# Kernel tuning notes

Measured on AMD Instinct MI355X. Metric: run time of the kernel, lower is better.

Reference implementation:

```python
import jax, jax.numpy as jnp
import numpy as np

NEG_INF = -1e30
EPS = 1e-6


def _apply_rope_interleaved(x, cos, sin):
    # x: (..., rope_dim); cos/sin broadcastable to (..., rope_dim//2)
    x1 = x[..., 0::2]
    x2 = x[..., 1::2]
    o1 = x1 * cos - x2 * sin
    o2 = x1 * sin + x2 * cos
    return jnp.stack([o1, o2], axis=-1).reshape(x.shape)


def setup_inputs() -> dict:
    key = jax.random.key(0)
    ks = jax.random.split(key, 6)
    B, S, D = 1, 2048, 7168
    H, HD, ROPE, QLR = 64, 128, 64, 1536
    x = jax.random.normal(ks[0], (B, S, D), dtype=jnp.float32)
    q_lora = jax.random.normal(ks[1], (B, S, QLR), dtype=jnp.float32)
    wq_b = jax.random.normal(ks[2], (QLR, H * HD), dtype=jnp.float32) * 0.02
    wk = jax.random.normal(ks[3], (D, HD), dtype=jnp.float32) * 0.02
    weights_proj = jax.random.normal(ks[4], (D, H), dtype=jnp.float32) * 0.02
    k_norm_w = jnp.ones((HD,), dtype=jnp.float32)
    k_norm_b = jnp.zeros((HD,), dtype=jnp.float32)
    # standard RoPE tables for the first ROPE dims
    half = ROPE // 2
    inv_freq = 1.0 / (10000.0 ** (np.arange(half, dtype=np.float64) / half))
    ang = np.arange(S, dtype=np.float64)[:, None] * inv_freq[None, :]
    cos = jnp.asarray(np.cos(ang), dtype=jnp.float32)
    sin = jnp.asarray(np.sin(ang), dtype=jnp.float32)
    return {"x": x, "q_lora": q_lora, "wq_b": wq_b, "wk": wk,
            "weights_proj": weights_proj, "k_norm_w": k_norm_w,
            "k_norm_b": k_norm_b, "cos": cos, "sin": sin, "topk": 512}


def reference(x, q_lora, wq_b, wk, weights_proj, k_norm_w, k_norm_b, cos, sin, topk):
    B, S, D = x.shape
    HD = wk.shape[1]
    H = weights_proj.shape[1]
    ROPE = cos.shape[1] * 2
    # queries: low-rank up-projection -> per-head, RoPE on first ROPE dims
    q = (q_lora @ wq_b).reshape(B, S, H, HD)
    q_pe = _apply_rope_interleaved(q[..., :ROPE], cos[None, :, None, :], sin[None, :, None, :])
    q = jnp.concatenate([q_pe, q[..., ROPE:]], axis=-1)
    # keys: single head, LayerNorm then RoPE on first ROPE dims
    k = x @ wk  # [B,S,HD]
    mu = k.mean(-1, keepdims=True)
    var = ((k - mu) ** 2).mean(-1, keepdims=True)
    k = (k - mu) * jax.lax.rsqrt(var + EPS) * k_norm_w + k_norm_b
    k_pe = _apply_rope_interleaved(k[..., :ROPE], cos[None], sin[None])
    k = jnp.concatenate([k_pe, k[..., ROPE:]], axis=-1)
    # per-token head gates, scaled by n_heads^-0.5 and softmax scale HD^-0.5
    w = (x @ weights_proj) * (H ** -0.5) * (HD ** -0.5)  # [B,S,H]
    # lightning index score: I[t,s] = sum_h w[t,h] * relu(q[t,h] . k[s])
    scores = jax.nn.relu(jnp.einsum('bshd,btd->bsht', q, k))  # [B,S,H,S]
    index_score = jnp.einsum('bsht,bsh->bst', scores, w)      # [B,S,S]
    # causal mask then top-k token selection
    causal = jnp.arange(S)[None, :] <= jnp.arange(S)[:, None]
    index_score = jnp.where(causal[None], index_score, NEG_INF)
    vals, idx = jax.lax.top_k(index_score, topk)
    return vals, idx
```

## Files before the change

### kernel.cpp

```cpp
#include <hip/hip_runtime.h>
#include <stdint.h>

#define S_LEN 2048
#define D_DIM 7168
#define H_NUM 64
#define HD_DIM 128
#define QLR_DIM 1536
#define NQ_DIM 8192
#define ROPE_DIM 64
#define HALF_DIM 32
#define TOPK_N 512
#define NEG_INF_F (-1e30f)
#define LN_EPS 1e-6f
#define W_SCALE 0.011048543456039806f

#define KCHUNKS 7
#define KCHUNK_SZ 1024
#define NKT 24

#define QF_HSTRIDE (128 * 4 * 64 * 8)

#define QBF_OFF 0
#define ALORA_OFF (QBF_OFF + S_LEN * NQ_DIM / 2)
#define WT_OFF   (ALORA_OFF + S_LEN * QLR_DIM / 2)
#define XBF_OFF  (WT_OFF + NQ_DIM * QLR_DIM / 2)
#define WT2_OFF  (XBF_OFF + S_LEN * D_DIM / 2)
#define KF_OFF   (WT2_OFF + 192 * D_DIM / 2)
#define KBF_OFF  (KF_OFF + S_LEN * HD_DIM)
#define WF_OFF   (KBF_OFF + S_LEN * HD_DIM / 2)
#define SC_OFF   (WF_OFF + S_LEN * H_NUM)

typedef __attribute__((ext_vector_type(8))) short short8;
typedef __attribute__((ext_vector_type(4))) float floatx4;

__device__ __forceinline__ ushort f2bf(float f) {
    unsigned int u = __float_as_uint(f);
    u += 0x7FFFu + ((u >> 16) & 1u);
    return (ushort)(u >> 16);
}
__device__ __forceinline__ unsigned int pack2bf(float lo, float hi) {
    return (unsigned int)f2bf(lo) | ((unsigned int)f2bf(hi) << 16);
}

__device__ __forceinline__ void gld_lds16(const ushort* g, ushort* l) {
    __builtin_amdgcn_global_load_lds(
        (const __attribute__((address_space(1))) unsigned int*)g,
        (__attribute__((address_space(3))) unsigned int*)l, 16, 0, 0);
}

__global__ __launch_bounds__(256) void cast_bf16_kernel(
    const float* __restrict__ in, ushort* __restrict__ out)
{
    int g = (blockIdx.x * 256 + threadIdx.x) * 8;
    float4 a = *(const float4*)&in[g];
    float4 b = *(const float4*)&in[g + 4];
    uint4 v;
    v.x = pack2bf(a.x, a.y); v.y = pack2bf(a.z, a.w);
    v.z = pack2bf(b.x, b.y); v.w = pack2bf(b.z, b.w);
    *(uint4*)&out[g] = v;
}

__global__ __launch_bounds__(256) void transpose_wqb_kernel(
    const float* __restrict__ W, ushort* __restrict__ WT)
{
    __shared__ ushort tl[64][72];
    const int n0 = blockIdx.x * 64, k0 = blockIdx.y * 64;
    const int t = threadIdx.x;
    const int r = t >> 4, c4 = (t & 15) * 4;
#pragma unroll
    for (int u = 0; u < 4; u++) {
        int kk = r + u * 16;
        float4 v = *(const float4*)&W[(size_t)(k0 + kk) * NQ_DIM + n0 + c4];
        tl[c4 + 0][kk] = f2bf(v.x);
        tl[c4 + 1][kk] = f2bf(v.y);
        tl[c4 + 2][kk] = f2bf(v.z);
        tl[c4 + 3][kk] = f2bf(v.w);
    }
    __syncthreads();
#pragma unroll
    for (int u = 0; u < 2; u++) {
        int i = t + u * 256;
        int nr = i >> 3, c8 = (i & 7) * 8;
        uint4 v = *(const uint4*)&tl[nr][c8];
        *(uint4*)&WT[(size_t)(n0 + nr) * QLR_DIM + k0 + c8] = v;
    }
}

__global__ __launch_bounds__(256) void transpose_wkp_kernel(
    const float* __restrict__ WK, const float* __restrict__ WP,
    ushort* __restrict__ WT2)
{
    __shared__ ushort tl[64][72];
    const int ntile = blockIdx.x;
    const int k0 = blockIdx.y * 64;
    const float* src; int ld, cbase;
    if (ntile < 2) { src = WK; ld = HD_DIM; cbase = ntile * 64; }
    else           { src = WP; ld = H_NUM; cbase = 0; }
    const int t = threadIdx.x;
    const int r = t >> 4, c4 = (t & 15) * 4;
#pragma unroll
    for (int u = 0; u < 4; u++) {
        int kk = r + u * 16;
        float4 v = *(const float4*)&src[(size_t)(k0 + kk) * ld + cbase + c4];
        tl[c4 + 0][kk] = f2bf(v.x);
        tl[c4 + 1][kk] = f2bf(v.y);
        tl[c4 + 2][kk] = f2bf(v.z);
        tl[c4 + 3][kk] = f2bf(v.w);
    }
    __syncthreads();
#pragma unroll
    for (int u = 0; u < 2; u++) {
        int i = t + u * 256;
        int nr = i >> 3, c8 = (i & 7) * 8;
        uint4 v = *(const uint4*)&tl[nr][c8];
        *(uint4*)&WT2[(size_t)(ntile * 64 + nr) * D_DIM + k0 + c8] = v;
    }
}

__global__ __launch_bounds__(512, 2) void qgemm_mfma_kernel(
    const ushort* __restrict__ Abf,
    const ushort* __restrict__ WT,
    const float* __restrict__ cosp, const float* __restrict__ sinp,
    ushort* __restrict__ Qo)
{
    __shared__ __align__(16) ushort lds[65536];

    const int tid = threadIdx.x;
    const int lane = tid & 63;
    const int wave = tid >> 6;
    const int m = lane & 15;
    const int q = lane >> 4;
    const int wm = wave & 1;
    const int wn = wave >> 1;

    const int wg = blockIdx.x;
    const int xcd = wg & 7, lid = wg >> 3;
    const int bx = xcd * 4 + (lid & 3);
    const int by = lid >> 2;
    const int m0 = by * 256;
    const int n0 = bx * 256;

    const ushort* sgA[2][2];
    const ushort* sgB[2][2];
    unsigned int ldoff[2][2];
#pragma unroll
    for (int h = 0; h < 2; h++)
#pragma unroll
        for (int r = 0; r < 2; r++) {
            int s = r * 512 + wave * 64 + lane;
            int row = s >> 3, c = s & 7;
            int kg = c ^ (row & 7);
            sgA[h][r] = Abf + (size_t)(m0 + h * 128 + row) * QLR_DIM + kg * 8;
            sgB[h][r] = WT  + (size_t)(n0 + h * 128 + row) * QLR_DIM + kg * 8;
            ldoff[h][r] = (unsigned int)(h * 8192 + (r * 512 + wave * 64) * 8);
        }

    auto stageA = [&](int kt, int h) {
        ushort* dbase = &lds[(kt & 1) * 16384];
        gld_lds16(sgA[h][0] + kt * 64, dbase + ldoff[h][0]);
        gld_lds16(sgA[h][1] + kt * 64, dbase + ldoff[h][1]);
    };
    auto stageB = [&](int kt, int h) {
        ushort* dbase = &lds[32768 + (kt & 1) * 16384];
        gld_lds16(sgB[h][0] + kt * 64, dbase + ldoff[h][0]);
        gld_lds16(sgB[h][1] + kt * 64, dbase + ldoff[h][1]);
    };

    unsigned int aoff[2], boff[2];
#pragma unroll
    for (int ks = 0; ks < 2; ks++) {
        unsigned int xr = (unsigned int)(((((ks << 2) + q) ^ (m & 7))) * 8);
        aoff[ks] = (unsigned int)((wm * 128 + m) * 64) + xr;
        boff[ks] = (unsigned int)((wn * 64 + m) * 64) + xr;
    }

    floatx4 acc[8][4];
#pragma unroll
    for (int i = 0; i < 8; i++)
#pragma unroll
        for (int j = 0; j < 4; j++) acc[i][j] = (floatx4){0.f, 0.f, 0.f, 0.f};

    stageA(0, 0); stageA(0, 1); stageB(0, 0); stageB(0, 1);
    asm volatile("s_waitcnt vmcnt(0)" ::: "memory");
    __builtin_amdgcn_s_barrier();

#pragma unroll 2
    for (int kt = 0; kt < NKT; ++kt) {
        const ushort* as = &lds[(kt & 1) * 16384];
        const ushort* bs = &lds[32768 + (kt & 1) * 16384];
        const bool pf = (kt + 1 < NKT);

        short8 af[4], bf0[4], bf1[4];

#pragma unroll
        for (int mt = 0; mt < 4; mt++)
            af[mt] = *(const short8*)&as[aoff[0] + mt * 1024];
#pragma unroll
        for (int nt = 0; nt < 4; nt++)
            bf0[nt] = *(const short8*)&bs[boff[0] + nt * 1024];
        if (pf) { stageA(kt + 1, 0); stageA(kt + 1, 1); stageB(kt + 1, 0); }
        __builtin_amdgcn_s_barrier();
        __builtin_amdgcn_s_setprio(1);
#pragma unroll
        for (int mt = 0; mt < 4; mt++)
#pragma unroll
            for (int nt = 0; nt < 4; nt++)
                acc[mt][nt] = __builtin_amdgcn_mfma_f32_16x16x32_bf16(
                    af[mt], bf0[nt], acc[mt][nt], 0, 0, 0);
        __builtin_amdgcn_s_setprio(0);
        __builtin_amdgcn_s_barrier();

#pragma unroll
        for (int mt = 0; mt < 4; mt++)
            af[mt] = *(const short8*)&as[aoff[1] + mt * 1024];
#pragma unroll
        for (int nt = 0; nt < 4; nt++)
            bf1[nt] = *(const short8*)&bs[boff[1] + nt * 1024];
        if (pf) stageB(kt + 1, 1);
        __builtin_amdgcn_s_barrier();
        __builtin_amdgcn_s_setprio(1);
#pragma unroll
        for (int mt = 0; mt < 4; mt++)
#pragma unroll
            for (int nt = 0; nt < 4; nt++)
                acc[mt][nt] = __builtin_amdgcn_mfma_f32_16x16x32_bf16(
                    af[mt], bf1[nt], acc[mt][nt], 0, 0, 0);
        __builtin_amdgcn_s_setprio(0);
        __builtin_amdgcn_s_barrier();

#pragma unroll
        for (int mt = 0; mt < 4; mt++)
            af[mt] = *(const short8*)&as[aoff[0] + 4096 + mt * 1024];
        __builtin_amdgcn_s_barrier();
        __builtin_amdgcn_s_setprio(1);
#pragma unroll
        for (int mt = 0; mt < 4; mt++)
#pragma unroll
            for (int nt = 0; nt < 4; nt++)
                acc[4 + mt][nt] = __builtin_amdgcn_mfma_f32_16x16x32_bf16(
                    af[mt], bf0[nt], acc[4 + mt][nt], 0, 0, 0);
        __builtin_amdgcn_s_setprio(0);
        __builtin_amdgcn_s_barrier();

#pragma unroll
        for (int mt = 0; mt < 4; mt++)
            af[mt] = *(const short8*)&as[aoff[1] + 4096 + mt * 1024];
        __builtin_amdgcn_s_barrier();
        __builtin_amdgcn_s_setprio(1);
#pragma unroll
        for (int mt = 0; mt < 4; mt++)
#pragma unroll
            for (int nt = 0; nt < 4; nt++)
                acc[4 + mt][nt] = __builtin_amdgcn_mfma_f32_16x16x32_bf16(
                    af[mt], bf1[nt], acc[4 + mt][nt], 0, 0, 0);
        __builtin_amdgcn_s_setprio(0);
        asm volatile("s_waitcnt vmcnt(0)" ::: "memory");
        __builtin_amdgcn_s_barrier();
    }

    __syncthreads();
    ushort* ep = lds;
    const int h0 = bx * 2;
    const int sgrp0 = m0 >> 4;

#pragma unroll
    for (int hh = 0; hh < 2; hh++) {
        if ((wn >> 1) == hh) {
            const int dbase = (wn & 1) * 64;
            const bool do_rope = ((wn & 1) == 0);
#pragma unroll
            for (int ai = 0; ai < 8; ai++) {
                const int srow0 = m0 + wm * 128 + ai * 16 + q * 4;
#pragma unroll
                for (int bj = 0; bj < 4; bj++) {
                    const int d = dbase + bj * 16 + m;
                    float o[4];
                    if (do_rope) {
                        const int jj = d >> 1;
#pragma unroll
                        for (int r = 0; r < 4; r++) {
                            float x = acc[ai][bj][r];
                            float p = __shfl_xor(x, 1, 64);
                            float c = cosp[(srow0 + r) * HALF_DIM + jj];
                            float sn = sinp[(srow0 + r) * HALF_DIM + jj];
                            o[r] = (d & 1) ? (p * sn + x * c) : (x * c - p * sn);
                        }
                    } else {
#pragma unroll
                        for (int r = 0; r < 4; r++) o[r] = acc[ai][bj][r];
                    }
#pragma unroll
                    for (int r = 0; r < 4; r++)
                        ep[(wm * 128 + ai * 16 + q * 4 + r) * 136 + d] = f2bf(o[r]);
                }
            }
        }
        __syncthreads();
        const size_t hstr = (size_t)(h0 + hh) * QF_HSTRIDE;
#pragma unroll
        for (int u = 0; u < 8; u++) {
            int i = u * 512 + tid;
            int sgl = i >> 8, c = i & 255;
            int ks = c >> 6, ln = c & 63;
            int srow = sgl * 16 + (ln & 15);
            int d0 = (ks << 5) + ((ln >> 4) << 3);
            uint4 v = *(const uint4*)&ep[srow * 136 + d0];
            *(uint4*)&Qo[hstr + ((((size_t)(sgrp0 + sgl) * 4 + ks) * 64 + ln) * 8)] = v;
        }
        __syncthreads();
    }
}

__global__ __launch_bounds__(256) void kw_mfma_kernel(
    const ushort* __restrict__ Xbf,
    const ushort* __restrict__ WT2,
    float* __restrict__ partial)
{
    __shared__ ushort As[128 * 64];
    __shared__ ushort Bs[64 * 64];

    const int tid = threadIdx.x;
    const int lane = tid & 63;
    const int wave = tid >> 6;
    const int m = lane & 15;
    const int q = lane >> 4;
    const int wm = wave & 1, wn = wave >> 1;
    const int m0 = blockIdx.x * 128;
    const int n0 = blockIdx.y * 64;
    const int kc = blockIdx.z;
    const size_t kbase = (size_t)kc * KCHUNK_SZ;

    const ushort* agp[4];
    unsigned int abase[4];
#pragma unroll
    for (int u = 0; u < 4; u++) {
        int s = (u * 4 + wave) * 64 + lane;
        int row = s >> 3, c = s & 7;
        int kg = c ^ (row & 7);
        agp[u] = Xbf + (size_t)(m0 + row) * D_DIM + kbase + kg * 8;
        abase[u] = (unsigned int)((u * 4 + wave) * 64 * 8);
    }
    const ushort* bgp[2];
    unsigned int bbase[2];
#pragma unroll
    for (int u = 0; u < 2; u++) {
        int s = (u * 4 + wave) * 64 + lane;
        int row = s >> 3, c = s & 7;
        int kg = c ^ (row & 7);
        bgp[u] = WT2 + (size_t)(n0 + row) * D_DIM + kbase + kg * 8;
        bbase[u] = (unsigned int)((u * 4 + wave) * 64 * 8);
    }

    floatx4 acc[4][2];
#pragma unroll
    for (int i = 0; i < 4; i++)
#pragma unroll
        for (int j = 0; j < 2; j++) acc[i][j] = (floatx4){0.f, 0.f, 0.f, 0.f};

    for (int kt = 0; kt < KCHUNK_SZ; kt += 64) {
        __syncthreads();
#pragma unroll
        for (int u = 0; u < 4; u++) gld_lds16(agp[u] + kt, &As[abase[u]]);
#pragma unroll
        for (int u = 0; u < 2; u++) gld_lds16(bgp[u] + kt, &Bs[bbase[u]]);
        __syncthreads();

        short8 af[4][2], bfr[2][2];
#pragma unroll
        for (int mt = 0; mt < 4; mt++) {
            int row = wm * 64 + mt * 16 + m;
#pragma unroll
            for (int ks = 0; ks < 2; ks++)
                af[mt][ks] = *(const short8*)
                    &As[row * 64 + ((((ks << 2) + q) ^ (m & 7)) * 8)];
        }
#pragma unroll
        for (int nt = 0; nt < 2; nt++) {
            int row = wn * 32 + nt * 16 + m;
#pragma unroll
            for (int ks = 0; ks < 2; ks++)
                bfr[nt][ks] = *(const short8*)
                    &Bs[row * 64 + ((((ks << 2) + q) ^ (m & 7)) * 8)];
        }
#pragma unroll
        for (int mt = 0; mt < 4; mt++)
#pragma unroll
            for (int nt = 0; nt < 2; nt++)
#pragma unroll
                for (int ks = 0; ks < 2; ks++)
                    acc[mt][nt] = __builtin_amdgcn_mfma_f32_16x16x32_bf16(
                        af[mt][ks], bfr[nt][ks], acc[mt][nt], 0, 0, 0);
    }

#pragma unroll
    for (int mt = 0; mt < 4; mt++) {
        int grow = m0 + wm * 64 + mt * 16 + q * 4;
#pragma unroll
        for (int nt = 0; nt < 2; nt++) {
            int gn = n0 + wn * 32 + nt * 16 + m;
#pragma unroll
            for (int r = 0; r < 4; r++)
                partial[((size_t)kc * S_LEN + grow + r) * 192 + gn] = acc[mt][nt][r];
        }
    }
}

__global__ __launch_bounds__(256) void kw_reduce_kernel(
    const float* __restrict__ partial, float* __restrict__ Ko, float* __restrict__ Wo)
{
    int g = blockIdx.x * 256 + threadIdx.x;
    int m = g / 192, n = g % 192;
    float s = 0.f;
#pragma unroll
    for (int c = 0; c < KCHUNKS; c++)
        s += partial[((size_t)c * S_LEN + m) * 192 + n];
    if (n < HD_DIM) Ko[(size_t)m * HD_DIM + n] = s;
    else            Wo[(size_t)m * H_NUM + (n - HD_DIM)] = s * W_SCALE;
}

__global__ __launch_bounds__(128) void knorm_rope_kernel(
    const float* __restrict__ Kf, const float* __restrict__ gw, const float* __restrict__ gb,
    const float* __restrict__ cosp, const float* __restrict__ sinp,
    ushort* __restrict__ Kbf)
{
    __shared__ float red[128];
    __shared__ float sh[128];
    const int m = blockIdx.x, t = threadIdx.x;
    float v = Kf[(size_t)m * HD_DIM + t];
    red[t] = v; __syncthreads();
    for (int off = 64; off > 0; off >>= 1) {
        if (t < off) red[t] += red[t + off];
        __syncthreads();
    }
    float mu = red[0] * (1.f / HD_DIM);
    __syncthreads();
    float dv = v - mu;
    red[t] = dv * dv; __syncthreads();
    for (int off = 64; off > 0; off >>= 1) {
        if (t < off) red[t] += red[t + off];
        __syncthreads();
    }
    float var = red[0] * (1.f / HD_DIM);
    float rs = rsqrtf(var + LN_EPS);
    float kn = dv * rs * gw[t] + gb[t];
    sh[t] = kn; __syncthreads();
    float out;
    if (t < ROPE_DIM) {
        int jj = t >> 1;
        float c = cosp[m * HALF_DIM + jj], sn = sinp[m * HALF_DIM + jj];
        out = ((t & 1) == 0) ? (sh[t] * c - sh[t + 1] * sn)
                             : (sh[t - 1] * sn + sh[t] * c);
    } else {
        out = kn;
    }
    Kbf[(size_t)m * HD_DIM + t] = f2bf(out);
}

__global__ __launch_bounds__(256, 2) void attn_mfma_kernel(
    const ushort* __restrict__ Qb,
    const ushort* __restrict__ Kb,
    const float* __restrict__ Wf,
    float* __restrict__ SC)
{
    __shared__ float Wsm[64 * 68];

    const int bidx = blockIdx.x;
    const int x = bidx & 7, j = bidx >> 3;
    const int g1 = x + 1, g2 = 32 - x, g3 = x + 9;
    int ts, tt;
    if (j < g1)                { ts = x;      tt = j; }
    else if (j < g1 + g2)      { ts = 31 - x; tt = j - g1; }
    else if (j < g1 + g2 + g3) { ts = x + 8;  tt = j - g1 - g2; }
    else                       { ts = 23 - x; tt = j - g1 - g2 - g3; }
    const int s0 = ts * 64, t0 = tt * 64;

    const int tid = threadIdx.x;
    const int lane = tid & 63;
    const int m = lane & 15;
    const int q = lane >> 4;
    const int strip = (tid >> 6) * 16;

    {
        const float4* gw = (const float4*)(Wf + (size_t)s0 * H_NUM);
#pragma unroll
        for (int u = 0; u < 4; u++) {
            int ch = tid + u * 256;
            float4 v = gw[ch];
            *(float4*)&Wsm[(ch >> 4) * 68 + (ch & 15) * 4] = v;
        }
    }

    short8 bf[4][4];
#pragma unroll
    for (int tile = 0; tile < 4; tile++)
#pragma unroll
        for (int ks = 0; ks < 4; ks++)
            bf[tile][ks] = *(const short8*)
                &Kb[(size_t)(t0 + tile * 16 + m) * HD_DIM + ks * 32 + q * 8];

    __syncthreads();

    float acc[4][4];
#pragma unroll
    for (int tile = 0; tile < 4; tile++)
#pragma unroll
        for (int r = 0; r < 4; r++) acc[tile][r] = 0.f;

    const int sgrp = ts * 4 + (strip >> 4);
    const ushort* qfb = Qb + ((size_t)sgrp * 4 * 64 + lane) * 8;
    const float* wrow = &Wsm[(strip + q * 4) * 68];

    auto loadQ = [&](short8* dst, int h) {
        const ushort* p = qfb + (size_t)h * QF_HSTRIDE;
#pragma unroll
        for (int ks = 0; ks < 4; ks++) dst[ks] = *(const short8*)&p[ks * 512];
    };
    auto computeH = [&](const short8* af, int h) {
        float wv[4];
#pragma unroll
        for (int r = 0; r < 4; r++) wv[r] = wrow[r * 68 + h];
#pragma unroll
        for (int tile = 0; tile < 4; tile++) {
            floatx4 p = {0.f, 0.f, 0.f, 0.f};
#pragma unroll
            for (int ks = 0; ks < 4; ks++)
                p = __builtin_amdgcn_mfma_f32_16x16x32_bf16(af[ks], bf[tile][ks], p, 0, 0, 0);
#pragma unroll
            for (int r = 0; r < 4; r++)
                acc[tile][r] += fmaxf(p[r], 0.f) * wv[r];
        }
    };

    short8 afA[4], afB[4];
    loadQ(afA, 0);
    for (int h = 0; h < H_NUM; h += 2) {
        loadQ(afB, h + 1);
        computeH(afA, h);
        if (h + 2 < H_NUM) loadQ(afA, h + 2);
        computeH(afB, h + 1);
    }

#pragma unroll
    for (int tile = 0; tile < 4; tile++)
#pragma unroll
        for (int r = 0; r < 4; r++)
            SC[(size_t)(s0 + strip + q * 4 + r) * S_LEN + t0 + tile * 16 + m] =
                acc[tile][r];
}

__device__ __forceinline__ unsigned int fkey(float f) {
    unsigned int u = __float_as_uint(f);
    return (u & 0x80000000u) ? ~u : (u | 0x80000000u);
}

__global__ __launch_bounds__(256) void topk_kernel(
    const float* __restrict__ SC, float* __restrict__ outv, float* __restrict__ outi)
{
    __shared__ unsigned int key[S_LEN];
    __shared__ float val[S_LEN];
    const int s = blockIdx.x, tid = threadIdx.x;
    const int nchunks = (s >> 9) + 1;
    const int nact = nchunks << 9;

    for (int t = tid; t < nact; t += 256) {
        float v = (t <= s) ? SC[(size_t)s * S_LEN + t] : NEG_INF_F;
        val[t] = v;
        key[t] = (fkey(v) & 0xFFFFF800u) | (unsigned int)(S_LEN - 1 - t);
    }
    __syncthreads();

    for (int k2 = 2; k2 <= 512; k2 <<= 1) {
        for (int j = k2 >> 1; j > 0; j >>= 1) {
            for (int p = tid; p < (nact >> 1); p += 256) {
                int i = 2 * p - (p & (j - 1));
                int il = i & 511;
                unsigned int a = key[i], b = key[i + j];
                bool up = ((il & k2) == 0);
                bool sw = up ? (a < b) : (a > b);
                if (sw) { key[i] = b; key[i + j] = a; }
            }
            __syncthreads();
        }
    }

    for (int c = 1; c < nchunks; c++) {
        for (int p = tid; p < 512; p += 256) {
            unsigned int a = key[p], b = key[(c << 9) + 511 - p];
            key[p] = a > b ? a : b;
        }
        __syncthreads();
        for (int j = 256; j > 0; j >>= 1) {
            int p = tid;
            int i = 2 * p - (p & (j - 1));
            unsigned int a = key[i], b = key[i + j];
            if (a < b) { key[i] = b; key[i + j] = a; }
            __syncthreads();
        }
    }

    for (int i2 = tid; i2 < TOPK_N; i2 += 256) {
        unsigned int kv = key[i2];
        int t = S_LEN - 1 - (int)(kv & 0x7FFu);
        outv[(size_t)s * TOPK_N + i2] = val[t];
        outi[(size_t)s * TOPK_N + i2] = (float)t;
    }
}

extern "C" void kernel_launch(void* const* d_in, const int* in_sizes, int n_in,
                              void* d_out, int out_size, void* d_ws, size_t ws_size,
                              hipStream_t stream)
{
    (void)in_sizes; (void)n_in; (void)out_size; (void)ws_size;
    const float* x      = (const float*)d_in[0];
    const float* q_lora = (const float*)d_in[1];
    const float* wq_b   = (const float*)d_in[2];
    const float* wk     = (const float*)d_in[3];
    const float* wproj  = (const float*)d_in[4];
    const float* knw    = (const float*)d_in[5];
    const float* knb    = (const float*)d_in[6];
    const float* cosp   = (const float*)d_in[7];
    const float* sinp   = (const float*)d_in[8];

    float* ws = (float*)d_ws;
    ushort* Qbf  = (ushort*)(ws + QBF_OFF);
    ushort* Albf = (ushort*)(ws + ALORA_OFF);
    ushort* WTbf = (ushort*)(ws + WT_OFF);
    ushort* Xbf  = (ushort*)(ws + XBF_OFF);
    ushort* WT2  = (ushort*)(ws + WT2_OFF);
    float*  Kf   = ws + KF_OFF;
    ushort* Kbf  = (ushort*)(ws + KBF_OFF);
    float*  Wf   = ws + WF_OFF;
    float*  SCb  = ws + SC_OFF;
    float*  partial = ws + SC_OFF;

    float* outv = (float*)d_out;
    float* outi = outv + (size_t)S_LEN * TOPK_N;

    cast_bf16_kernel<<<(S_LEN * QLR_DIM) / (256 * 8), 256, 0, stream>>>(q_lora, Albf);
    cast_bf16_kernel<<<(S_LEN * D_DIM) / (256 * 8), 256, 0, stream>>>(x, Xbf);
    transpose_wqb_kernel<<<dim3(NQ_DIM / 64, QLR_DIM / 64), 256, 0, stream>>>(wq_b, WTbf);
    transpose_wkp_kernel<<<dim3(3, D_DIM / 64), 256, 0, stream>>>(wk, wproj, WT2);
    kw_mfma_kernel<<<dim3(S_LEN / 128, 3, KCHUNKS), 256, 0, stream>>>(Xbf, WT2, partial);
    kw_reduce_kernel<<<(S_LEN * 192) / 256, 256, 0, stream>>>(partial, Kf, Wf);
    knorm_rope_kernel<<<S_LEN, 128, 0, stream>>>(Kf, knw, knb, cosp, sinp, Kbf);
    qgemm_mfma_kernel<<<256, 512, 0, stream>>>(Albf, WTbf, cosp, sinp, Qbf);
    attn_mfma_kernel<<<528, 256, 0, stream>>>(Qbf, Kbf, Wf, SCb);
    topk_kernel<<<S_LEN, 256, 0, stream>>>(SCb, outv, outi);
}
```

Before: 340.0 us.

## Simplify Q GEMM pipeline and double-buffer K/W projection GEMM

```diff
diff --git a/kernel.cpp b/kernel.cpp
--- a/kernel.cpp
+++ b/kernel.cpp
@@ -155,15 +155,17 @@
             ldoff[h][r] = (unsigned int)(h * 8192 + (r * 512 + wave * 64) * 8);
         }
 
-    auto stageA = [&](int kt, int h) {
-        ushort* dbase = &lds[(kt & 1) * 16384];
-        gld_lds16(sgA[h][0] + kt * 64, dbase + ldoff[h][0]);
-        gld_lds16(sgA[h][1] + kt * 64, dbase + ldoff[h][1]);
-    };
-    auto stageB = [&](int kt, int h) {
-        ushort* dbase = &lds[32768 + (kt & 1) * 16384];
-        gld_lds16(sgB[h][0] + kt * 64, dbase + ldoff[h][0]);
-        gld_lds16(sgB[h][1] + kt * 64, dbase + ldoff[h][1]);
+    auto stageAll = [&](int kt) {
+        ushort* da = &lds[(kt & 1) * 16384];
+        ushort* db = &lds[32768 + (kt & 1) * 16384];
+        gld_lds16(sgA[0][0] + kt * 64, da + ldoff[0][0]);
+        gld_lds16(sgA[0][1] + kt * 64, da + ldoff[0][1]);
+        gld_lds16(sgA[1][0] + kt * 64, da + ldoff[1][0]);
+        gld_lds16(sgA[1][1] + kt * 64, da + ldoff[1][1]);
+        gld_lds16(sgB[0][0] + kt * 64, db + ldoff[0][0]);
+        gld_lds16(sgB[0][1] + kt * 64, db + ldoff[0][1]);
+        gld_lds16(sgB[1][0] + kt * 64, db + ldoff[1][0]);
+        gld_lds16(sgB[1][1] + kt * 64, db + ldoff[1][1]);
     };
 
     unsigned int aoff[2], boff[2];
@@ -180,85 +182,66 @@
 #pragma unroll
         for (int j = 0; j < 4; j++) acc[i][j] = (floatx4){0.f, 0.f, 0.f, 0.f};
 
-    stageA(0, 0); stageA(0, 1); stageB(0, 0); stageB(0, 1);
-    asm volatile("s_waitcnt vmcnt(0)" ::: "memory");
-    __builtin_amdgcn_s_barrier();
+    stageAll(0);
+    __syncthreads();
 
 #pragma unroll 2
     for (int kt = 0; kt < NKT; ++kt) {
         const ushort* as = &lds[(kt & 1) * 16384];
         const ushort* bs = &lds[32768 + (kt & 1) * 16384];
-        const bool pf = (kt + 1 < NKT);
+        if (kt + 1 < NKT) stageAll(kt + 1);
 
         short8 af[4], bf0[4], bf1[4];
 
-#pragma unroll
-        for (int mt = 0; mt < 4; mt++)
-            af[mt] = *(const short8*)&as[aoff[0] + mt * 1024];
 #pragma unroll
         for (int nt = 0; nt < 4; nt++)
             bf0[nt] = *(const short8*)&bs[boff[0] + nt * 1024];
-        if (pf) { stageA(kt + 1, 0); stageA(kt + 1, 1); stageB(kt + 1, 0); }
-        __builtin_amdgcn_s_barrier();
-        __builtin_amdgcn_s_setprio(1);
+#pragma unroll
+        for (int mt = 0; mt < 4; mt++)
+            af[mt] = *(const short8*)&as[aoff[0] + mt * 1024];
 #pragma unroll
         for (int mt = 0; mt < 4; mt++)
 #pragma unroll
             for (int nt = 0; nt < 4; nt++)
                 acc[mt][nt] = __builtin_amdgcn_mfma_f32_16x16x32_bf16(
                     af[mt], bf0[nt], acc[mt][nt], 0, 0, 0);
-        __builtin_amdgcn_s_setprio(0);
-        __builtin_amdgcn_s_barrier();
-
-#pragma unroll
-        for (int mt = 0; mt < 4; mt++)
-            af[mt] = *(const short8*)&as[aoff[1] + mt * 1024];
+
+#pragma unroll
+        for (int mt = 0; mt < 4; mt++)
+            af[mt] = *(const short8*)&as[aoff[0] + 4096 + mt * 1024];
+#pragma unroll
+        for (int mt = 0; mt < 4; mt++)
+#pragma unroll
+            for (int nt = 0; nt < 4; nt++)
+                acc[4 + mt][nt] = __builtin_amdgcn_mfma_f32_16x16x32_bf16(
+                    af[mt], bf0[nt], acc[4 + mt][nt], 0, 0, 0);
+
 #pragma unroll
         for (int nt = 0; nt < 4; nt++)
             bf1[nt] = *(const short8*)&bs[boff[1] + nt * 1024];
-        if (pf) stageB(kt + 1, 1);
-        __builtin_amdgcn_s_barrier();
-        __builtin_amdgcn_s_setprio(1);
+#pragma unroll
+        for (int mt = 0; mt < 4; mt++)
+            af[mt] = *(const short8*)&as[aoff[1] + mt * 1024];
 #pragma unroll
         for (int mt = 0; mt < 4; mt++)
 #pragma unroll
             for (int nt = 0; nt < 4; nt++)
                 acc[mt][nt] = __builtin_amdgcn_mfma_f32_16x16x32_bf16(
                     af[mt], bf1[nt], acc[mt][nt], 0, 0, 0);
-        __builtin_amdgcn_s_setprio(0);
-        __builtin_amdgcn_s_barrier();
-
-#pragma unroll
-        for (int mt = 0; mt < 4; mt++)
-            af[mt] = *(const short8*)&as[aoff[0] + 4096 + mt * 1024];
-        __builtin_amdgcn_s_barrier();
-        __builtin_amdgcn_s_setprio(1);
-#pragma unroll
-        for (int mt = 0; mt < 4; mt++)
-#pragma unroll
-            for (int nt = 0; nt < 4; nt++)
-                acc[4 + mt][nt] = __builtin_amdgcn_mfma_f32_16x16x32_bf16(
-                    af[mt], bf0[nt], acc[4 + mt][nt], 0, 0, 0);
-        __builtin_amdgcn_s_setprio(0);
-        __builtin_amdgcn_s_barrier();
 
 #pragma unroll
         for (int mt = 0; mt < 4; mt++)
             af[mt] = *(const short8*)&as[aoff[1] + 4096 + mt * 1024];
-        __builtin_amdgcn_s_barrier();
-        __builtin_amdgcn_s_setprio(1);
 #pragma unroll
         for (int mt = 0; mt < 4; mt++)
 #pragma unroll
             for (int nt = 0; nt < 4; nt++)
                 acc[4 + mt][nt] = __builtin_amdgcn_mfma_f32_16x16x32_bf16(
                     af[mt], bf1[nt], acc[4 + mt][nt], 0, 0, 0);
-        __builtin_amdgcn_s_setprio(0);
-        asm volatile("s_waitcnt vmcnt(0)" ::: "memory");
-        __builtin_amdgcn_s_barrier();
-    }
-
-    __syncthreads();
+
+        __syncthreads();
+    }
+
     ushort* ep = lds;
     const int h0 = bx * 2;
     const int sgrp0 = m0 >> 4;
@@ -270,7 +253,8 @@
             const bool do_rope = ((wn & 1) == 0);
 #pragma unroll
             for (int ai = 0; ai < 8; ai++) {
-                const int srow0 = m0 + wm * 128 + ai * 16 + q * 4;
+                const int srow0 = m0 + wm * 128 + (ai & 3) * 16 + (ai >> 2) * 64 + q * 4;
+                const int lrow0 = srow0 - m0;
 #pragma unroll
                 for (int bj = 0; bj < 4; bj++) {
                     const int d = dbase + bj * 16 + m;
@@ -279,7 +263,7 @@
                         const int jj = d >> 1;
 #pragma unroll
                         for (int r = 0; r < 4; r++) {
-                            float x = acc[ai][bj][r];
+                            float x = acc[(ai >> 2) * 4 + (ai & 3)][bj][r];
                             float p = __shfl_xor(x, 1, 64);
                             float c = cosp[(srow0 + r) * HALF_DIM + jj];
                             float sn = sinp[(srow0 + r) * HALF_DIM + jj];
@@ -287,11 +271,12 @@
                         }
                     } else {
 #pragma unroll
-                        for (int r = 0; r < 4; r++) o[r] = acc[ai][bj][r];
+                        for (int r = 0; r < 4; r++)
+                            o[r] = acc[(ai >> 2) * 4 + (ai & 3)][bj][r];
                     }
 #pragma unroll
                     for (int r = 0; r < 4; r++)
-                        ep[(wm * 128 + ai * 16 + q * 4 + r) * 136 + d] = f2bf(o[r]);
+                        ep[(lrow0 + r) * 136 + d] = f2bf(o[r]);
                 }
             }
         }
@@ -316,8 +301,8 @@
     const ushort* __restrict__ WT2,
     float* __restrict__ partial)
 {
-    __shared__ ushort As[128 * 64];
-    __shared__ ushort Bs[64 * 64];
+    __shared__ ushort As[2 * 128 * 64];
+    __shared__ ushort Bs[2 * 64 * 64];
 
     const int tid = threadIdx.x;
     const int lane = tid & 63;
@@ -351,19 +336,29 @@
         bbase[u] = (unsigned int)((u * 4 + wave) * 64 * 8);
     }
 
+    auto stage = [&](int t) {
+        ushort* da = &As[(t & 1) * 8192];
+        ushort* db = &Bs[(t & 1) * 4096];
+#pragma unroll
+        for (int u = 0; u < 4; u++) gld_lds16(agp[u] + t * 64, da + abase[u]);
+#pragma unroll
+        for (int u = 0; u < 2; u++) gld_lds16(bgp[u] + t * 64, db + bbase[u]);
+    };
+
     floatx4 acc[4][2];
 #pragma unroll
     for (int i = 0; i < 4; i++)
 #pragma unroll
         for (int j = 0; j < 2; j++) acc[i][j] = (floatx4){0.f, 0.f, 0.f, 0.f};
 
-    for (int kt = 0; kt < KCHUNK_SZ; kt += 64) {
-        __syncthreads();
-#pragma unroll
-        for (int u = 0; u < 4; u++) gld_lds16(agp[u] + kt, &As[abase[u]]);
-#pragma unroll
-        for (int u = 0; u < 2; u++) gld_lds16(bgp[u] + kt, &Bs[bbase[u]]);
-        __syncthreads();
+    stage(0);
+    __syncthreads();
+
+#pragma unroll 2
+    for (int t = 0; t < KCHUNK_SZ / 64; ++t) {
+        const ushort* as = &As[(t & 1) * 8192];
+        const ushort* bs = &Bs[(t & 1) * 4096];
+        if (t + 1 < KCHUNK_SZ / 64) stage(t + 1);
 
         short8 af[4][2], bfr[2][2];
 #pragma unroll
@@ -372,7 +367,7 @@
 #pragma unroll
             for (int ks = 0; ks < 2; ks++)
                 af[mt][ks] = *(const short8*)
-                    &As[row * 64 + ((((ks << 2) + q) ^ (m & 7)) * 8)];
+                    &as[row * 64 + ((((ks << 2) + q) ^ (m & 7)) * 8)];
         }
 #pragma unroll
         for (int nt = 0; nt < 2; nt++) {
@@ -380,7 +375,7 @@
 #pragma unroll
             for (int ks = 0; ks < 2; ks++)
                 bfr[nt][ks] = *(const short8*)
-                    &Bs[row * 64 + ((((ks << 2) + q) ^ (m & 7)) * 8)];
+                    &bs[row * 64 + ((((ks << 2) + q) ^ (m & 7)) * 8)];
         }
 #pragma unroll
         for (int mt = 0; mt < 4; mt++)
@@ -390,6 +385,8 @@
                 for (int ks = 0; ks < 2; ks++)
                     acc[mt][nt] = __builtin_amdgcn_mfma_f32_16x16x32_bf16(
                         af[mt][ks], bfr[nt][ks], acc[mt][nt], 0, 0, 0);
+
+        __syncthreads();
     }
 
 #pragma unroll
```

New measurement: 339.4 us. About the same (-0.2%).
